# Optimization experiments

Hardware: AMD Instinct MI355X
Metric: run time of the kernel (lower is better)

## Reference

```python
import jax, jax.numpy as jnp
import numpy as np

B, T, F, H = 64, 512, 512, 1024


def setup_inputs() -> dict:
    key = jax.random.key(0)
    k1, k2, k3 = jax.random.split(key, 3)
    x = jax.random.normal(k1, (B, T, F), dtype=jnp.float32)
    c0 = jnp.zeros((B, H), dtype=jnp.float32)
    h0 = jnp.zeros((B, H), dtype=jnp.float32)
    # Flax LSTMCell: input projection (no bias) + hidden projection (with bias),
    # fused here into [4H]-wide kernels with gate order (i, f, g, o).
    Wi = jax.random.normal(k2, (F, 4 * H), dtype=jnp.float32) / np.sqrt(F)
    Wh = jax.random.normal(k3, (H, 4 * H), dtype=jnp.float32) / np.sqrt(H)
    bh = jnp.zeros((4 * H,), dtype=jnp.float32)
    return {"x": x, "c0": c0, "h0": h0, "Wi": Wi, "Wh": Wh, "bh": bh}


def reference(x, c0, h0, Wi, Wh, bh):
    # Precompute input projections for the whole sequence in one big GEMM.
    # zx: (T, B, 4H)
    zx = jnp.einsum('btf,fg->tbg', x, Wi)

    def step(carry, zx_t):
        c, h = carry
        z = zx_t + h @ Wh + bh  # (B, 4H)
        i, f, g, o = jnp.split(z, 4, axis=-1)
        i = jax.nn.sigmoid(i)
        f = jax.nn.sigmoid(f)
        g = jnp.tanh(g)
        o = jax.nn.sigmoid(o)
        c_new = f * c + i * g
        h_new = o * jnp.tanh(c_new)
        return (c_new, h_new), h_new

    (_, _), ys = jax.lax.scan(step, (c0, h0), zx)
    return jnp.swapaxes(ys, 0, 1)  # (B, T, H)
```

## Files before the change

kernel.cpp:

```cpp
#include <hip/hip_runtime.h>

#define Bdim 64
#define Tdim 512
#define Fdim 512
#define Hdim 1024
#define NKB  48
#define NXKB 16
#define NHKB 32
#define NWG  128
#define NTHR 512

typedef __attribute__((ext_vector_type(8))) _Float16     f16x8;
typedef __attribute__((ext_vector_type(4))) float        f32x4;
typedef __attribute__((ext_vector_type(4))) unsigned int u32x4;

#define MFMA(a, b, c) __builtin_amdgcn_mfma_f32_16x16x32_f16((a), (b), (c), 0, 0, 0)

#define WP_ELEMS    (256*48*64*8)
#define BIAS_OFF    ((size_t)WP_ELEMS * 2)
#define HBUF_OFF    (BIAS_OFF + 4096 * 4)
#define SLOT_BYTES  131072
#define NRING       513
#define FLAG_OFF    (HBUF_OFF + (size_t)NRING * SLOT_BYTES)
#define FLAG_STRIDE 32

__device__ __forceinline__ float sigmoidf_(float v) {
    return 1.0f / (1.0f + __expf(-v));
}
__device__ __forceinline__ float tanhf_(float v) {
    return 1.0f - 2.0f / (1.0f + __expf(2.0f * v));
}

__device__ __forceinline__ f16x8 uload16_l2(const void* p) {
    f16x8 r;
    asm volatile("global_load_dwordx4 %0, %1, off sc0"
                 : "=v"(r) : "v"(p) : "memory");
    return r;
}
__device__ __forceinline__ void ustore16(void* p, f32x4 v) {
    asm volatile("global_store_dwordx4 %0, %1, off sc0 sc1"
                 :: "v"(p), "v"(v) : "memory");
}

#define WAITV(N) do { asm volatile("s_waitcnt vmcnt(" #N ")" ::: "memory"); \
                      __builtin_amdgcn_sched_barrier(0); } while (0)

__global__ void pack_w_kernel(const float* __restrict__ Wi, const float* __restrict__ Wh,
                              _Float16* __restrict__ Wp)
{
    int d = blockIdx.x * blockDim.x + threadIdx.x;
    int tn   = d / 3072;
    int r    = d % 3072;
    int kb   = r / 64;
    int lane = r % 64;
    int kg = lane >> 4, lm = lane & 15;
    int Np = tn * 16 + lm;
    int g    = Np >> 5;
    int lc   = Np & 31;
    int gate = lc >> 3, c = lc & 7;
    int n  = gate * Hdim + g * 8 + c;
    int k0 = kb * 32 + kg * 8;
    f16x8 v;
#pragma unroll
    for (int j = 0; j < 8; ++j) {
        int k = k0 + j;
        float w = (k < Fdim) ? Wi[(long)k * 4096 + n] : Wh[(long)(k - Fdim) * 4096 + n];
        v[j] = (_Float16)w;
    }
    ((f16x8*)Wp)[d] = v;
}

__global__ void pack_misc_kernel(const float* __restrict__ bh, const float* __restrict__ h0,
                                 float* __restrict__ bias_p, _Float16* __restrict__ hbuf,
                                 unsigned int* __restrict__ flags)
{
    int t = blockIdx.x * blockDim.x + threadIdx.x;
    if (t < NWG) flags[t * FLAG_STRIDE] = 0u;
    if (t < 4096) {
        int g = t >> 5, lc = t & 31;
        int gate = lc >> 3, c = lc & 7;
        bias_p[t] = bh[gate * Hdim + g * 8 + c];
    }
    {
        int wgp = t >> 9;
        int b   = (t >> 3) & 63;
        int c   = t & 7;
        hbuf[t] = (_Float16)h0[b * Hdim + wgp * 8 + c];
    }
}

__global__ __launch_bounds__(NTHR, 1)
void lstm_kernel(const float* __restrict__ x, const float* __restrict__ c0,
                 const f16x8* __restrict__ Wp8, const float* __restrict__ bias_p,
                 _Float16* __restrict__ hbuf, unsigned int* __restrict__ flags,
                 float* __restrict__ out)
{
    __shared__ f16x8 wlds[2 * NKB * 64];
    __shared__ float zlds[Bdim][33];
    __shared__ float zxlds[2][Bdim][33];

    const int wg    = (blockIdx.x & 7) * 16 + (blockIdx.x >> 3);
    const int tid   = threadIdx.x;
    const int wave  = tid >> 6;
    const int lane  = tid & 63;
    const int kg    = lane >> 4;
    const int lm    = lane & 15;
    const bool isH  = (wave < 4);
    const int  rt   = isH ? wave : (wave - 4);

    {
        const f16x8* src = Wp8 + (size_t)wg * 2 * NKB * 64;
        for (int e = tid; e < 2 * NKB * 64; e += NTHR) wlds[e] = src[e];
    }

    const float bias0 = bias_p[wg * 32 + lm];
    const float bias1 = bias_p[wg * 32 + 16 + lm];

    const int grow = (wave & 3) * 16 + (lane >> 2);
    const int gjl  = (lane & 3) * 2;
    float cc0 = 0.f, cc1 = 0.f;
    if (isH) {
        cc0 = c0[grow * Hdim + wg * 8 + gjl];
        cc1 = c0[grow * Hdim + wg * 8 + gjl + 1];
    }

    const int arow = rt * 16 + lm;
    const float* __restrict__ xrow = x + (size_t)arow * Tdim * Fdim + kg * 8;

    char* __restrict__ hb  = (char*)hbuf;
    const char* __restrict__ hrd = hb + (size_t)kg * 1024 + (size_t)arow * 16;
    const size_t mypkt = (size_t)wg * 1024 + (size_t)grow * 16;

#define XPHASE(TT, BUF)                                                     \
    {                                                                       \
        const float* xt = xrow + (size_t)(TT) * Fdim;                       \
        f32x4 xa0 = {0.f, 0.f, 0.f, 0.f};                                   \
        f32x4 xa1 = {0.f, 0.f, 0.f, 0.f};                                   \
        _Pragma("unroll 8")                                                 \
        for (int kb = 0; kb < NXKB; ++kb) {                                 \
            const f32x4* ap = (const f32x4*)(xt + kb * 32);                 \
            f32x4 lo = ap[0];                                               \
            f32x4 hi = ap[1];                                               \
            f16x8 a;                                                        \
            _Pragma("unroll")                                               \
            for (int j = 0; j < 4; ++j) { a[j] = (_Float16)lo[j]; a[4+j] = (_Float16)hi[j]; } \
            xa0 = MFMA(a, wlds[kb * 64 + lane], xa0);                       \
            xa1 = MFMA(a, wlds[NKB * 64 + kb * 64 + lane], xa1);            \
        }                                                                   \
        int rbase = rt * 16 + kg * 4;                                       \
        _Pragma("unroll")                                                   \
        for (int r = 0; r < 4; ++r) {                                       \
            zxlds[BUF][rbase + r][lm]      = xa0[r];                        \
            zxlds[BUF][rbase + r][16 + lm] = xa1[r];                        \
        }                                                                   \
    }

    if (!isH) XPHASE(0, 0);
    __syncthreads();

    for (int t = 0; t < Tdim; ++t) {
        if (isH) {
            f32x4 acc0a = {bias0, bias0, bias0, bias0};
            f32x4 acc1a = {bias1, bias1, bias1, bias1};
            f32x4 acc0b = {0.f, 0.f, 0.f, 0.f};
            f32x4 acc1b = {0.f, 0.f, 0.f, 0.f};
            {
                const char* hq = hrd + (size_t)t * SLOT_BYTES;
                f16x8 hA[8], hB[8], hC[8], hD[8];

#define HLOAD(BASE, H)                                                  \
                _Pragma("unroll")                                       \
                for (int k = 0; k < 8; ++k)                             \
                    H[k] = uload16_l2(hq + (size_t)((BASE) + k) * 4096);

#define HGROUP(BASE, H)                                                 \
                _Pragma("unroll")                                       \
                for (int k = 0; k < 8; ++k) {                           \
                    int kb = (BASE) + k;                                \
                    f16x8 bf0 = wlds[(NXKB + kb) * 64 + lane];          \
                    f16x8 bf1 = wlds[NKB * 64 + (NXKB + kb) * 64 + lane]; \
                    if (kb & 1) { acc0b = MFMA(H[k], bf0, acc0b); acc1b = MFMA(H[k], bf1, acc1b); } \
                    else        { acc0a = MFMA(H[k], bf0, acc0a); acc1a = MFMA(H[k], bf1, acc1a); } \
                }

                HLOAD(0,  hA);
                HLOAD(8,  hB);
                HLOAD(16, hC);
                HLOAD(24, hD);
                WAITV(24);
                HGROUP(0,  hA);
                WAITV(16);
                HGROUP(8,  hB);
                WAITV(8);
                HGROUP(16, hC);
                WAITV(0);
                HGROUP(24, hD);
#undef HLOAD
#undef HGROUP
            }
            {
                const int buf = t & 1;
                int rbase = rt * 16 + kg * 4;
#pragma unroll
                for (int r = 0; r < 4; ++r) {
                    float z0 = acc0a[r] + acc0b[r] + zxlds[buf][rbase + r][lm];
                    float z1 = acc1a[r] + acc1b[r] + zxlds[buf][rbase + r][16 + lm];
                    zlds[rbase + r][lm]      = z0;
                    zlds[rbase + r][16 + lm] = z1;
                }
            }
            asm volatile("s_waitcnt lgkmcnt(0)" ::: "memory");
            __builtin_amdgcn_sched_barrier(0);

            float hv0, hv1;
            {
                float i0 = sigmoidf_(zlds[grow][gjl]);
                float f0 = sigmoidf_(zlds[grow][8 + gjl]);
                float g0 = tanhf_(zlds[grow][16 + gjl]);
                float o0 = sigmoidf_(zlds[grow][24 + gjl]);
                cc0 = f0 * cc0 + i0 * g0;
                hv0 = o0 * tanhf_(cc0);

                float i1 = sigmoidf_(zlds[grow][gjl + 1]);
                float f1 = sigmoidf_(zlds[grow][8 + gjl + 1]);
                float g1 = tanhf_(zlds[grow][16 + gjl + 1]);
                float o1 = sigmoidf_(zlds[grow][24 + gjl + 1]);
                cc1 = f1 * cc1 + i1 * g1;
                hv1 = o1 * tanhf_(cc1);
            }

            {
                union { _Float16 h[2]; unsigned int u; } pk;
                pk.h[0] = (_Float16)hv0; pk.h[1] = (_Float16)hv1;
                const int lb = lane & ~3;
                unsigned int q0 = __shfl(pk.u, lb);
                unsigned int q1 = __shfl(pk.u, lb + 1);
                unsigned int q2 = __shfl(pk.u, lb + 2);
                unsigned int q3 = __shfl(pk.u, lb + 3);
                if (!(lane & 3)) {
                    u32x4 pkt = {q0, q1, q2, q3};
                    ustore16(hb + (size_t)(t + 1) * SLOT_BYTES + mypkt,
                             __builtin_bit_cast(f32x4, pkt));
                }
            }
            asm volatile("s_waitcnt vmcnt(0)" ::: "memory");
            if (lane == 0)
                __hip_atomic_fetch_add(flags + (size_t)wg * FLAG_STRIDE, 1u,
                                       __ATOMIC_RELAXED, __HIP_MEMORY_SCOPE_AGENT);

            {
                float2 ov; ov.x = hv0; ov.y = hv1;
                *(float2*)(out + ((size_t)grow * Tdim + t) * Hdim + wg * 8 + gjl) = ov;
            }
        } else {
            {
                const int tn  = (t + 1 < Tdim) ? (t + 1) : t;
                const int buf = (t + 1) & 1;
                XPHASE(tn, buf);
            }
            asm volatile("s_waitcnt lgkmcnt(0)" ::: "memory");

            if (wave == 4 && t + 1 < Tdim) {
                const unsigned int target = 4u * (unsigned int)(t + 1);
                while (true) {
                    unsigned int f0 = __hip_atomic_load(flags + (size_t)lane * FLAG_STRIDE,
                                                        __ATOMIC_RELAXED, __HIP_MEMORY_SCOPE_AGENT);
                    unsigned int f1 = __hip_atomic_load(flags + (size_t)(64 + lane) * FLAG_STRIDE,
                                                        __ATOMIC_RELAXED, __HIP_MEMORY_SCOPE_AGENT);
                    if (__all(f0 >= target && f1 >= target)) break;
                    __builtin_amdgcn_s_sleep(1);
                }
            }
        }
        __builtin_amdgcn_s_barrier();
    }
#undef XPHASE
}

extern "C" void kernel_launch(void* const* d_in, const int* in_sizes, int n_in,
                              void* d_out, int out_size, void* d_ws, size_t ws_size,
                              hipStream_t stream)
{
    const float* x  = (const float*)d_in[0];
    const float* c0 = (const float*)d_in[1];
    const float* h0 = (const float*)d_in[2];
    const float* Wi = (const float*)d_in[3];
    const float* Wh = (const float*)d_in[4];
    const float* bh = (const float*)d_in[5];
    float* out = (float*)d_out;

    char* ws = (char*)d_ws;
    _Float16*     Wp     = (_Float16*)(ws);
    float*        bias_p = (float*)(ws + BIAS_OFF);
    _Float16*     hbuf   = (_Float16*)(ws + HBUF_OFF);
    unsigned int* flags  = (unsigned int*)(ws + FLAG_OFF);

    hipLaunchKernelGGL(pack_w_kernel,    dim3(3072), dim3(256), 0, stream, Wi, Wh, Wp);
    hipLaunchKernelGGL(pack_misc_kernel, dim3(256),  dim3(256), 0, stream, bh, h0, bias_p, hbuf, flags);
    hipLaunchKernelGGL(lstm_kernel, dim3(NWG), dim3(NTHR), 0, stream,
                       x, c0, (const f16x8*)Wp, bias_p, hbuf, flags, out);
}
```

Measured before the change: 3.187 ms.

## Replace per-step workgroup barrier with fine-grained LDS token gating per h-chunk

Removes the per-timestep s_barrier and instead uses LDS tokens: the polling wave publishes readiness per quarter of producer workgroups, so H waves can start loading h chunks as soon as their producers have posted. Producer/consumer tokens also guard the double-buffered zx LDS between x-projection waves and h waves. This aims to overlap h loads with the tail of the grid-wide wait and to decouple wave groups, at the cost of spin loops on LDS and weaker ordering guarantees between waves.

```diff
diff --git a/kernel.cpp b/kernel.cpp
--- a/kernel.cpp
+++ b/kernel.cpp
@@ -44,6 +44,13 @@
 
 #define WAITV(N) do { asm volatile("s_waitcnt vmcnt(" #N ")" ::: "memory"); \
                       __builtin_amdgcn_sched_barrier(0); } while (0)
+
+__device__ __forceinline__ unsigned ldtok(const unsigned* p) {
+    return __hip_atomic_load(p, __ATOMIC_RELAXED, __HIP_MEMORY_SCOPE_WORKGROUP);
+}
+__device__ __forceinline__ void sttok(unsigned* p, unsigned v) {
+    __hip_atomic_store(p, v, __ATOMIC_RELAXED, __HIP_MEMORY_SCOPE_WORKGROUP);
+}
 
 __global__ void pack_w_kernel(const float* __restrict__ Wi, const float* __restrict__ Wh,
                               _Float16* __restrict__ Wp)
@@ -98,6 +105,9 @@
     __shared__ f16x8 wlds[2 * NKB * 64];
     __shared__ float zlds[Bdim][33];
     __shared__ float zxlds[2][Bdim][33];
+    __shared__ unsigned gateT[4];
+    __shared__ unsigned prodDone[4];
+    __shared__ unsigned consDone[4];
 
     const int wg    = (blockIdx.x & 7) * 16 + (blockIdx.x >> 3);
     const int tid   = threadIdx.x;
@@ -112,6 +122,7 @@
         const f16x8* src = Wp8 + (size_t)wg * 2 * NKB * 64;
         for (int e = tid; e < 2 * NKB * 64; e += NTHR) wlds[e] = src[e];
     }
+    if (tid < 4) { gateT[tid] = 0; prodDone[tid] = 0; consDone[tid] = 0; }
 
     const float bias0 = bias_p[wg * 32 + lm];
     const float bias1 = bias_p[wg * 32 + 16 + lm];
@@ -157,6 +168,7 @@
 
     if (!isH) XPHASE(0, 0);
     __syncthreads();
+    if (!isH && lane == 0) sttok(&prodDone[rt], 1u);
 
     for (int t = 0; t < Tdim; ++t) {
         if (isH) {
@@ -167,6 +179,10 @@
             {
                 const char* hq = hrd + (size_t)t * SLOT_BYTES;
                 f16x8 hA[8], hB[8], hC[8], hD[8];
+
+#define HGATE(G)                                                        \
+                if (t) { while (ldtok(&gateT[G]) < (unsigned)t)         \
+                             __builtin_amdgcn_s_sleep(1); }
 
 #define HLOAD(BASE, H)                                                  \
                 _Pragma("unroll")                                       \
@@ -183,22 +199,25 @@
                     else        { acc0a = MFMA(H[k], bf0, acc0a); acc1a = MFMA(H[k], bf1, acc1a); } \
                 }
 
-                HLOAD(0,  hA);
-                HLOAD(8,  hB);
-                HLOAD(16, hC);
-                HLOAD(24, hD);
-                WAITV(24);
+                HGATE(0); HLOAD(0,  hA);
+                HGATE(1); HLOAD(8,  hB);
+                WAITV(8);
                 HGROUP(0,  hA);
-                WAITV(16);
+                HGATE(2); HLOAD(16, hC);
+                WAITV(8);
                 HGROUP(8,  hB);
+                HGATE(3); HLOAD(24, hD);
                 WAITV(8);
                 HGROUP(16, hC);
                 WAITV(0);
                 HGROUP(24, hD);
+#undef HGATE
 #undef HLOAD
 #undef HGROUP
             }
             {
+                while (ldtok(&prodDone[rt]) < (unsigned)(t + 1))
+                    __builtin_amdgcn_s_sleep(1);
                 const int buf = t & 1;
                 int rbase = rt * 16 + kg * 4;
 #pragma unroll
@@ -211,6 +230,7 @@
             }
             asm volatile("s_waitcnt lgkmcnt(0)" ::: "memory");
             __builtin_amdgcn_sched_barrier(0);
+            if (lane == 0) sttok(&consDone[rt], (unsigned)(t + 1));
 
             float hv0, hv1;
             {
@@ -243,36 +263,57 @@
                              __builtin_bit_cast(f32x4, pkt));
                 }
             }
-            asm volatile("s_waitcnt vmcnt(0)" ::: "memory");
+            WAITV(0);
             if (lane == 0)
                 __hip_atomic_fetch_add(flags + (size_t)wg * FLAG_STRIDE, 1u,
                                        __ATOMIC_RELAXED, __HIP_MEMORY_SCOPE_AGENT);
-
             {
                 float2 ov; ov.x = hv0; ov.y = hv1;
                 *(float2*)(out + ((size_t)grow * Tdim + t) * Hdim + wg * 8 + gjl) = ov;
             }
         } else {
             {
+                if (t) {
+                    while (ldtok(&consDone[rt]) < (unsigned)t)
+                        __builtin_amdgcn_s_sleep(1);
+                }
                 const int tn  = (t + 1 < Tdim) ? (t + 1) : t;
                 const int buf = (t + 1) & 1;
                 XPHASE(tn, buf);
             }
             asm volatile("s_waitcnt lgkmcnt(0)" ::: "memory");
+            if (lane == 0) sttok(&prodDone[rt], (unsigned)(t + 2));
 
             if (wave == 4 && t + 1 < Tdim) {
-                const unsigned int target = 4u * (unsigned int)(t + 1);
-                while (true) {
-                    unsigned int f0 = __hip_atomic_load(flags + (size_t)lane * FLAG_STRIDE,
-                                                        __ATOMIC_RELAXED, __HIP_MEMORY_SCOPE_AGENT);
-                    unsigned int f1 = __hip_atomic_load(flags + (size_t)(64 + lane) * FLAG_STRIDE,
-                                                        __ATOMIC_RELAXED, __HIP_MEMORY_SCOPE_AGENT);
-                    if (__all(f0 >= target && f1 >= target)) break;
-                    __builtin_amdgcn_s_sleep(1);
+                const unsigned tgt = 4u * (unsigned)(t + 1);
+                unsigned posted = 0;
+                while (posted != 0xFu) {
+                    unsigned f0 = __hip_atomic_load(flags + (size_t)lane * FLAG_STRIDE,
+                                                    __ATOMIC_RELAXED, __HIP_MEMORY_SCOPE_AGENT);
+                    unsigned f1 = __hip_atomic_load(flags + (size_t)(64 + lane) * FLAG_STRIDE,
+                                                    __ATOMIC_RELAXED, __HIP_MEMORY_SCOPE_AGENT);
+                    unsigned long long b0 = __ballot(f0 >= tgt);
+                    unsigned long long b1 = __ballot(f1 >= tgt);
+                    if (!(posted & 1u) && (unsigned)b0 == 0xFFFFFFFFu) {
+                        if (lane == 0) sttok(&gateT[0], (unsigned)(t + 1));
+                        posted |= 1u;
+                    }
+                    if (!(posted & 2u) && (unsigned)(b0 >> 32) == 0xFFFFFFFFu) {
+                        if (lane == 0) sttok(&gateT[1], (unsigned)(t + 1));
+                        posted |= 2u;
+                    }
+                    if (!(posted & 4u) && (unsigned)b1 == 0xFFFFFFFFu) {
+                        if (lane == 0) sttok(&gateT[2], (unsigned)(t + 1));
+                        posted |= 4u;
+                    }
+                    if (!(posted & 8u) && (unsigned)(b1 >> 32) == 0xFFFFFFFFu) {
+                        if (lane == 0) sttok(&gateT[3], (unsigned)(t + 1));
+                        posted |= 8u;
+                    }
+                    if (posted != 0xFu) __builtin_amdgcn_s_sleep(1);
                 }
             }
         }
-        __builtin_amdgcn_s_barrier();
     }
 #undef XPHASE
 }
```

New measurement: 3.147 ms (median of 2 runs). About the same (-1.2%).

## Replace global flag barrier with sentinel-tagged h ring and intra-WG tokens

Applied to the files above, without the earlier changes.

Drops the per-step global atomic flag counters and polling wave. Consumers now detect readiness from the h data itself, using an all-ones sentinel written into a 4-slot ring that is invalidated two steps ahead. The per-step workgroup s_barrier is replaced by LDS producer/consumer tokens between the x-projection waves and the recurrent waves. This removes a store-wait-atomic-poll round trip from the critical path. In exchange, correctness depends on fp16 h values never matching the sentinel pattern and on the ordering of the sentinel and data stores.

```diff
diff --git a/kernel.cpp b/kernel.cpp
--- a/kernel.cpp
+++ b/kernel.cpp
@@ -20,9 +20,7 @@
 #define BIAS_OFF    ((size_t)WP_ELEMS * 2)
 #define HBUF_OFF    (BIAS_OFF + 4096 * 4)
 #define SLOT_BYTES  131072
-#define NRING       513
-#define FLAG_OFF    (HBUF_OFF + (size_t)NRING * SLOT_BYTES)
-#define FLAG_STRIDE 32
+#define SLOT_HALVES 65536
 
 __device__ __forceinline__ float sigmoidf_(float v) {
     return 1.0f / (1.0f + __expf(-v));
@@ -31,9 +29,9 @@
     return 1.0f - 2.0f / (1.0f + __expf(2.0f * v));
 }
 
-__device__ __forceinline__ f16x8 uload16_l2(const void* p) {
+__device__ __forceinline__ f16x8 uload16(const void* p) {
     f16x8 r;
-    asm volatile("global_load_dwordx4 %0, %1, off sc0"
+    asm volatile("global_load_dwordx4 %0, %1, off sc0 sc1"
                  : "=v"(r) : "v"(p) : "memory");
     return r;
 }
@@ -44,6 +42,19 @@
 
 #define WAITV(N) do { asm volatile("s_waitcnt vmcnt(" #N ")" ::: "memory"); \
                       __builtin_amdgcn_sched_barrier(0); } while (0)
+
+__device__ __forceinline__ bool stale8(f16x8 v) {
+    u32x4 u = __builtin_bit_cast(u32x4, v);
+    return (u[0] == 0xFFFFFFFFu) | (u[1] == 0xFFFFFFFFu) |
+           (u[2] == 0xFFFFFFFFu) | (u[3] == 0xFFFFFFFFu);
+}
+
+__device__ __forceinline__ unsigned ldtok(const unsigned* p) {
+    return __hip_atomic_load(p, __ATOMIC_RELAXED, __HIP_MEMORY_SCOPE_WORKGROUP);
+}
+__device__ __forceinline__ void sttok(unsigned* p, unsigned v) {
+    __hip_atomic_store(p, v, __ATOMIC_RELAXED, __HIP_MEMORY_SCOPE_WORKGROUP);
+}
 
 __global__ void pack_w_kernel(const float* __restrict__ Wi, const float* __restrict__ Wh,
                               _Float16* __restrict__ Wp)
@@ -71,11 +82,9 @@
 }
 
 __global__ void pack_misc_kernel(const float* __restrict__ bh, const float* __restrict__ h0,
-                                 float* __restrict__ bias_p, _Float16* __restrict__ hbuf,
-                                 unsigned int* __restrict__ flags)
+                                 float* __restrict__ bias_p, _Float16* __restrict__ hbuf)
 {
     int t = blockIdx.x * blockDim.x + threadIdx.x;
-    if (t < NWG) flags[t * FLAG_STRIDE] = 0u;
     if (t < 4096) {
         int g = t >> 5, lc = t & 31;
         int gate = lc >> 3, c = lc & 7;
@@ -87,17 +96,23 @@
         int c   = t & 7;
         hbuf[t] = (_Float16)h0[b * Hdim + wgp * 8 + c];
     }
+    {
+        unsigned int* up = (unsigned int*)(hbuf + SLOT_HALVES);
+        up[t] = 0xFFFFFFFFu;
+        if (t < 32768) up[65536 + t] = 0xFFFFFFFFu;
+    }
 }
 
 __global__ __launch_bounds__(NTHR, 1)
 void lstm_kernel(const float* __restrict__ x, const float* __restrict__ c0,
                  const f16x8* __restrict__ Wp8, const float* __restrict__ bias_p,
-                 _Float16* __restrict__ hbuf, unsigned int* __restrict__ flags,
-                 float* __restrict__ out)
+                 _Float16* __restrict__ hbuf, float* __restrict__ out)
 {
     __shared__ f16x8 wlds[2 * NKB * 64];
     __shared__ float zlds[Bdim][33];
     __shared__ float zxlds[2][Bdim][33];
+    __shared__ unsigned prodDone[4];
+    __shared__ unsigned consDone[4];
 
     const int wg    = (blockIdx.x & 7) * 16 + (blockIdx.x >> 3);
     const int tid   = threadIdx.x;
@@ -112,6 +127,7 @@
         const f16x8* src = Wp8 + (size_t)wg * 2 * NKB * 64;
         for (int e = tid; e < 2 * NKB * 64; e += NTHR) wlds[e] = src[e];
     }
+    if (tid < 4) { prodDone[tid] = 0; consDone[tid] = 0; }
 
     const float bias0 = bias_p[wg * 32 + lm];
     const float bias1 = bias_p[wg * 32 + 16 + lm];
@@ -157,21 +173,45 @@
 
     if (!isH) XPHASE(0, 0);
     __syncthreads();
+    if (!isH && lane == 0) sttok(&prodDone[rt], 1u);
 
     for (int t = 0; t < Tdim; ++t) {
         if (isH) {
+            if (!(lane & 3)) {
+                u32x4 sv = {0xFFFFFFFFu, 0xFFFFFFFFu, 0xFFFFFFFFu, 0xFFFFFFFFu};
+                ustore16(hb + (size_t)((t + 2) & 3) * SLOT_BYTES + mypkt,
+                         __builtin_bit_cast(f32x4, sv));
+            }
+
             f32x4 acc0a = {bias0, bias0, bias0, bias0};
             f32x4 acc1a = {bias1, bias1, bias1, bias1};
             f32x4 acc0b = {0.f, 0.f, 0.f, 0.f};
             f32x4 acc1b = {0.f, 0.f, 0.f, 0.f};
             {
-                const char* hq = hrd + (size_t)t * SLOT_BYTES;
+                const char* hq = hrd + (size_t)(t & 3) * SLOT_BYTES;
                 f16x8 hA[8], hB[8], hC[8], hD[8];
 
 #define HLOAD(BASE, H)                                                  \
                 _Pragma("unroll")                                       \
                 for (int k = 0; k < 8; ++k)                             \
-                    H[k] = uload16_l2(hq + (size_t)((BASE) + k) * 4096);
+                    H[k] = uload16(hq + (size_t)((BASE) + k) * 4096);
+
+#define HCHECK(BASE, H)                                                 \
+                {                                                       \
+                    bool st[8]; bool any = false;                       \
+                    _Pragma("unroll")                                   \
+                    for (int k = 0; k < 8; ++k) { st[k] = stale8(H[k]); any |= st[k]; } \
+                    while (__any(any)) {                                \
+                        __builtin_amdgcn_s_sleep(1);                    \
+                        _Pragma("unroll")                               \
+                        for (int k = 0; k < 8; ++k)                     \
+                            if (st[k]) H[k] = uload16(hq + (size_t)((BASE) + k) * 4096); \
+                        WAITV(0);                                       \
+                        any = false;                                    \
+                        _Pragma("unroll")                               \
+                        for (int k = 0; k < 8; ++k) { st[k] = stale8(H[k]); any |= st[k]; } \
+                    }                                                   \
+                }
 
 #define HGROUP(BASE, H)                                                 \
                 _Pragma("unroll")                                       \
@@ -188,17 +228,20 @@
                 HLOAD(16, hC);
                 HLOAD(24, hD);
                 WAITV(24);
-                HGROUP(0,  hA);
+                HCHECK(0,  hA);  HGROUP(0,  hA);
                 WAITV(16);
-                HGROUP(8,  hB);
+                HCHECK(8,  hB);  HGROUP(8,  hB);
                 WAITV(8);
-                HGROUP(16, hC);
+                HCHECK(16, hC);  HGROUP(16, hC);
                 WAITV(0);
-                HGROUP(24, hD);
+                HCHECK(24, hD);  HGROUP(24, hD);
 #undef HLOAD
+#undef HCHECK
 #undef HGROUP
             }
             {
+                while (ldtok(&prodDone[rt]) < (unsigned)(t + 1))
+                    __builtin_amdgcn_s_sleep(1);
                 const int buf = t & 1;
                 int rbase = rt * 16 + kg * 4;
 #pragma unroll
@@ -211,6 +254,7 @@
             }
             asm volatile("s_waitcnt lgkmcnt(0)" ::: "memory");
             __builtin_amdgcn_sched_barrier(0);
+            if (lane == 0) sttok(&consDone[rt], (unsigned)(t + 1));
 
             float hv0, hv1;
             {
@@ -239,40 +283,27 @@
                 unsigned int q3 = __shfl(pk.u, lb + 3);
                 if (!(lane & 3)) {
                     u32x4 pkt = {q0, q1, q2, q3};
-                    ustore16(hb + (size_t)(t + 1) * SLOT_BYTES + mypkt,
+                    ustore16(hb + (size_t)((t + 1) & 3) * SLOT_BYTES + mypkt,
                              __builtin_bit_cast(f32x4, pkt));
                 }
             }
-            asm volatile("s_waitcnt vmcnt(0)" ::: "memory");
-            if (lane == 0)
-                __hip_atomic_fetch_add(flags + (size_t)wg * FLAG_STRIDE, 1u,
-                                       __ATOMIC_RELAXED, __HIP_MEMORY_SCOPE_AGENT);
-
             {
                 float2 ov; ov.x = hv0; ov.y = hv1;
                 *(float2*)(out + ((size_t)grow * Tdim + t) * Hdim + wg * 8 + gjl) = ov;
             }
         } else {
+            if (t) {
+                while (ldtok(&consDone[rt]) < (unsigned)t)
+                    __builtin_amdgcn_s_sleep(1);
+            }
             {
                 const int tn  = (t + 1 < Tdim) ? (t + 1) : t;
                 const int buf = (t + 1) & 1;
                 XPHASE(tn, buf);
             }
             asm volatile("s_waitcnt lgkmcnt(0)" ::: "memory");
-
-            if (wave == 4 && t + 1 < Tdim) {
-                const unsigned int target = 4u * (unsigned int)(t + 1);
-                while (true) {
-                    unsigned int f0 = __hip_atomic_load(flags + (size_t)lane * FLAG_STRIDE,
-                                                        __ATOMIC_RELAXED, __HIP_MEMORY_SCOPE_AGENT);
-                    unsigned int f1 = __hip_atomic_load(flags + (size_t)(64 + lane) * FLAG_STRIDE,
-                                                        __ATOMIC_RELAXED, __HIP_MEMORY_SCOPE_AGENT);
-                    if (__all(f0 >= target && f1 >= target)) break;
-                    __builtin_amdgcn_s_sleep(1);
-                }
-            }
+            if (lane == 0) sttok(&prodDone[rt], (unsigned)(t + 2));
         }
-        __builtin_amdgcn_s_barrier();
     }
 #undef XPHASE
 }
@@ -290,13 +321,12 @@
     float* out = (float*)d_out;
 
     char* ws = (char*)d_ws;
-    _Float16*     Wp     = (_Float16*)(ws);
-    float*        bias_p = (float*)(ws + BIAS_OFF);
-    _Float16*     hbuf   = (_Float16*)(ws + HBUF_OFF);
-    unsigned int* flags  = (unsigned int*)(ws + FLAG_OFF);
+    _Float16* Wp     = (_Float16*)(ws);
+    float*    bias_p = (float*)(ws + BIAS_OFF);
+    _Float16* hbuf   = (_Float16*)(ws + HBUF_OFF);
 
     hipLaunchKernelGGL(pack_w_kernel,    dim3(3072), dim3(256), 0, stream, Wi, Wh, Wp);
-    hipLaunchKernelGGL(pack_misc_kernel, dim3(256),  dim3(256), 0, stream, bh, h0, bias_p, hbuf, flags);
+    hipLaunchKernelGGL(pack_misc_kernel, dim3(256),  dim3(256), 0, stream, bh, h0, bias_p, hbuf);
     hipLaunchKernelGGL(lstm_kernel, dim3(NWG), dim3(NTHR), 0, stream,
-                       x, c0, (const f16x8*)Wp, bias_p, hbuf, flags, out);
-}
+                       x, c0, (const f16x8*)Wp, bias_p, hbuf, out);
+}
```

New measurement: 4.161 ms. +30.6%, slower.
